# Kernel optimization log

Measured on AMD Instinct MI355X. Metric: run time of the kernel, lower is better.

Reference implementation:

```python
import jax, jax.numpy as jnp
import numpy as np

N_NODES = 100000
N_EDGES = 1600000
D = 128
N_CLASS = 10
N_LAYERS = 5
BN_EPS = 1e-5


def setup_inputs() -> dict:
    key = jax.random.key(0)
    ks = jax.random.split(key, 8)
    x = jax.random.normal(ks[0], (N_NODES, D), dtype=jnp.float32)
    edge_index = jax.random.randint(ks[1], (2, N_EDGES), 0, N_NODES, dtype=jnp.int32)
    s = 0.05  # small init scale for numerical stability through 5 layers
    W1 = jax.random.normal(ks[2], (N_LAYERS, D, D), dtype=jnp.float32) * s
    b1 = jnp.zeros((N_LAYERS, D), jnp.float32)
    gamma = jnp.ones((N_LAYERS, D), jnp.float32)
    beta = jnp.zeros((N_LAYERS, D), jnp.float32)
    mean = jnp.zeros((N_LAYERS, D), jnp.float32)
    var = jnp.ones((N_LAYERS, D), jnp.float32)
    W2 = jax.random.normal(ks[3], (N_LAYERS, D, D), dtype=jnp.float32) * s
    b2 = jnp.zeros((N_LAYERS, D), jnp.float32)
    lin1_w = jax.random.normal(ks[4], (D, D), dtype=jnp.float32) * s
    lin1_b = jnp.zeros((D,), jnp.float32)
    lin2_w = jax.random.normal(ks[5], (D, N_CLASS), dtype=jnp.float32) * s
    lin2_b = jnp.zeros((N_CLASS,), jnp.float32)
    return {"x": x, "edge_index": edge_index, "W1": W1, "b1": b1,
            "gamma": gamma, "beta": beta, "mean": mean, "var": var,
            "W2": W2, "b2": b2, "lin1_w": lin1_w, "lin1_b": lin1_b,
            "lin2_w": lin2_w, "lin2_b": lin2_b}


def reference(x, edge_index, W1, b1, gamma, beta, mean, var, W2, b2,
              lin1_w, lin1_b, lin2_w, lin2_b):
    n = x.shape[0]
    src, dst = edge_index[0], edge_index[1]
    h = x
    for l in range(N_LAYERS):
        # GIN aggregation: (1+eps)*h + sum_{j->i} h_j, eps=0 (GINConv default)
        agg = jax.ops.segment_sum(h[src], dst, num_segments=n)
        z = (h + agg) @ W1[l] + b1[l]
        # BatchNorm1d in eval mode (running stats)
        z = (z - mean[l]) * (gamma[l] / jnp.sqrt(var[l] + BN_EPS)) + beta[l]
        z = jax.nn.relu(z)
        h = jax.nn.relu(z @ W2[l] + b2[l])
    h = jax.nn.relu(h @ lin1_w + lin1_b)  # dropout is identity in eval
    h = h @ lin2_w + lin2_b
    return jax.nn.log_softmax(h, axis=1)
```

## Files before the change

### kernel.cpp

```cpp
#include <hip/hip_runtime.h>
#include <hip/hip_bf16.h>

#define DD 128
#define CAP 64

typedef __attribute__((ext_vector_type(8))) short short8;
typedef __attribute__((ext_vector_type(4))) float f32x4;

__device__ __forceinline__ float bf2f(short s) {
    union { unsigned u; float f; } c; c.u = ((unsigned)(unsigned short)s) << 16; return c.f;
}
__device__ __forceinline__ short f2bf(float f) {
    union { float f; unsigned u; } c; c.f = f;
    unsigned u = c.u + 0x7fffu + ((c.u >> 16) & 1u);
    return (short)(u >> 16);
}

__device__ __forceinline__ void gload_lds16(const void* g, void* l) {
    __builtin_amdgcn_global_load_lds(
        (const __attribute__((address_space(1))) unsigned int*)g,
        (__attribute__((address_space(3))) unsigned int*)l, 16, 0, 0);
}

__global__ __launch_bounds__(256) void f2b_k(
    const float* __restrict__ x, ushort* __restrict__ o, int n8)
{
    int i = blockIdx.x * 256 + threadIdx.x;
    if (i < n8) {
        float4 v0 = ((const float4*)x)[(size_t)i * 2];
        float4 v1 = ((const float4*)x)[(size_t)i * 2 + 1];
        short8 r;
        r[0] = f2bf(v0.x); r[1] = f2bf(v0.y); r[2] = f2bf(v0.z); r[3] = f2bf(v0.w);
        r[4] = f2bf(v1.x); r[5] = f2bf(v1.y); r[6] = f2bf(v1.z); r[7] = f2bf(v1.w);
        ((short8*)o)[i] = r;
    }
}

__global__ __launch_bounds__(256) void wconv_k(
    const float* __restrict__ W1, const float* __restrict__ W2,
    const float* __restrict__ L1, ushort* __restrict__ Wt)
{
    int idx = blockIdx.x * 256 + threadIdx.x;
    int mat = idx >> 14;
    if (mat >= 11) return;
    int e = idx & 16383;
    int k = e >> 7, n = e & 127;
    const float* src = (mat < 5) ? (W1 + (size_t)mat * 16384)
                     : (mat < 10) ? (W2 + (size_t)(mat - 5) * 16384) : L1;
    float v = src[e];
    int di = (n * 128 + k) ^ ((n & 7) << 3);
    Wt[(size_t)mat * 16384 + di] = (ushort)f2bf(v);
}

__global__ __launch_bounds__(256) void lin2conv_k(
    const float* __restrict__ w, ushort* __restrict__ L2t)
{
    int idx = blockIdx.x * 256 + threadIdx.x;
    if (idx >= 2048) return;
    int c = idx >> 7, k = idx & 127;
    float v = (c < 10) ? w[k * 10 + c] : 0.f;
    L2t[idx] = (ushort)f2bf(v);
}

#define RANGE_SUB 256
__global__ __launch_bounds__(256) void fill_k(
    const int* __restrict__ src, const int* __restrict__ dst,
    int* __restrict__ len, int* __restrict__ csr, int nEdges, int n)
{
    const int r    = blockIdx.x & 7;
    const int sub  = blockIdx.x >> 3;
    const int step = (n + 7) / 8;
    const int rlo  = r * step;
    const int rhi  = min(n, rlo + step);

    for (int base = sub * 1024; base < nEdges; base += RANGE_SUB * 1024) {
        int e0 = base + threadIdx.x * 4;
        if (e0 + 3 < nEdges) {
            int4 d = *(const int4*)(dst + e0);
            int4 s = *(const int4*)(src + e0);
            if (d.x >= rlo && d.x < rhi) { int i = atomicAdd(&len[d.x], 1); if (i < CAP) csr[(d.x << 6) + i] = s.x; }
            if (d.y >= rlo && d.y < rhi) { int i = atomicAdd(&len[d.y], 1); if (i < CAP) csr[(d.y << 6) + i] = s.y; }
            if (d.z >= rlo && d.z < rhi) { int i = atomicAdd(&len[d.z], 1); if (i < CAP) csr[(d.z << 6) + i] = s.z; }
            if (d.w >= rlo && d.w < rhi) { int i = atomicAdd(&len[d.w], 1); if (i < CAP) csr[(d.w << 6) + i] = s.w; }
        } else {
            for (int e = e0; e < nEdges; ++e) {
                int d = dst[e];
                if (d >= rlo && d < rhi) { int i = atomicAdd(&len[d], 1); if (i < CAP) csr[(d << 6) + i] = src[e]; }
            }
        }
    }
}

__global__ __launch_bounds__(256) void gather_bf_k(
    const ushort* __restrict__ h, const int* __restrict__ len,
    const int* __restrict__ csr, ushort* __restrict__ out, int n)
{
    int node = blockIdx.x * 16 + (threadIdx.x >> 4);
    int j = threadIdx.x & 15;
    if (node >= n) return;
    int beg = node << 6;
    int end = beg + min(len[node], CAP);
    const short8* hp = (const short8*)h;

    float a[8], b[8];
    short8 v = hp[(size_t)node * 16 + j];
#pragma unroll
    for (int i = 0; i < 8; ++i) { a[i] = bf2f(v[i]); b[i] = 0.f; }

    int k = beg;
    for (; k + 7 < end; k += 8) {
        int s0 = csr[k],     s1 = csr[k + 1], s2 = csr[k + 2], s3 = csr[k + 3];
        int s4 = csr[k + 4], s5 = csr[k + 5], s6 = csr[k + 6], s7 = csr[k + 7];
        short8 v0 = hp[(size_t)s0 * 16 + j];
        short8 v1 = hp[(size_t)s1 * 16 + j];
        short8 v2 = hp[(size_t)s2 * 16 + j];
        short8 v3 = hp[(size_t)s3 * 16 + j];
        short8 v4 = hp[(size_t)s4 * 16 + j];
        short8 v5 = hp[(size_t)s5 * 16 + j];
        short8 v6 = hp[(size_t)s6 * 16 + j];
        short8 v7 = hp[(size_t)s7 * 16 + j];
#pragma unroll
        for (int i = 0; i < 8; ++i) {
            a[i] += (bf2f(v0[i]) + bf2f(v1[i])) + (bf2f(v2[i]) + bf2f(v3[i]));
            b[i] += (bf2f(v4[i]) + bf2f(v5[i])) + (bf2f(v6[i]) + bf2f(v7[i]));
        }
    }
    if (k + 3 < end) {
        int s0 = csr[k], s1 = csr[k + 1], s2 = csr[k + 2], s3 = csr[k + 3];
        short8 v0 = hp[(size_t)s0 * 16 + j];
        short8 v1 = hp[(size_t)s1 * 16 + j];
        short8 v2 = hp[(size_t)s2 * 16 + j];
        short8 v3 = hp[(size_t)s3 * 16 + j];
#pragma unroll
        for (int i = 0; i < 8; ++i)
            a[i] += (bf2f(v0[i]) + bf2f(v1[i])) + (bf2f(v2[i]) + bf2f(v3[i]));
        k += 4;
    }
    for (; k < end; ++k) {
        int s0 = csr[k];
        short8 v0 = hp[(size_t)s0 * 16 + j];
#pragma unroll
        for (int i = 0; i < 8; ++i) b[i] += bf2f(v0[i]);
    }
    short8 r;
#pragma unroll
    for (int i = 0; i < 8; ++i) r[i] = f2bf(a[i] + b[i]);
    ((short8*)out)[(size_t)node * 16 + j] = r;
}

template <bool BN, int MODE>
__global__ __launch_bounds__(256, 2) void layer_k(
    const ushort* __restrict__ A, const ushort* __restrict__ W1t,
    const float* __restrict__ bias1,
    const float* __restrict__ gamma, const float* __restrict__ beta,
    const float* __restrict__ mean, const float* __restrict__ var,
    const ushort* __restrict__ W2t, const float* __restrict__ bias2,
    ushort* __restrict__ O, float* __restrict__ OUT, int nrows)
{
    __shared__ ushort sA[16384];
    __shared__ ushort sW[16384];
    const int tid  = threadIdx.x;
    const int row0 = blockIdx.x * 128;

    const int lane = tid & 63;
    const int wv   = tid >> 6;
    const int m0   = wv * 32;
    const int lr   = lane & 15;
    const int lg   = lane >> 4;

    short8 w2s[8];
    short8 b2f[4];
    if (MODE == 1) {
#pragma unroll
        for (int i = 0; i < 8; ++i)
            w2s[i] = ((const short8*)W2t)[i * 256 + tid];
    } else {
#pragma unroll
        for (int kk = 0; kk < 4; ++kk)
            b2f[kk] = *(const short8*)(W2t + lr * 128 + kk * 32 + lg * 8);
    }

#pragma unroll
    for (int i = 0; i < 8; ++i)
        gload_lds16(W1t + (i * 256 + tid) * 8, sW + (i * 256 + tid) * 8);
#pragma unroll
    for (int i = 0; i < 8; ++i) {
        int f  = i * 256 + tid;
        int r  = f >> 4;
        int c8 = f & 15;
        int gr = row0 + r;
        gload_lds16(A + (size_t)gr * DD + ((c8 ^ (r & 7)) * 8), sA + f * 8);
    }
    __syncthreads();

    float mul8[8], add8[8];
#pragma unroll
    for (int cf = 0; cf < 8; ++cf) {
        int n = cf * 16 + lr;
        if (BN) {
            float s = gamma[n] * rsqrtf(var[n] + 1e-5f);
            mul8[cf] = s;
            add8[cf] = (bias1[n] - mean[n]) * s + beta[n];
        } else {
            mul8[cf] = 1.f;
            add8[cf] = bias1[n];
        }
    }

    f32x4 acc[2][8];
#pragma unroll
    for (int rf = 0; rf < 2; ++rf)
#pragma unroll
        for (int cf = 0; cf < 8; ++cf) acc[rf][cf] = (f32x4){0.f, 0.f, 0.f, 0.f};

#pragma unroll
    for (int kk = 0; kk < 4; ++kk) {
        const int kb = kk * 64 + lg * 16;
        int ra0 = m0 + lr;
        int ra1 = m0 + 16 + lr;
        short8 a0 = *(short8*)((char*)sA + ((ra0 * 256 + kb) ^ ((ra0 & 7) << 4)));
        short8 a1 = *(short8*)((char*)sA + ((ra1 * 256 + kb) ^ ((ra1 & 7) << 4)));
        short8 b[8];
#pragma unroll
        for (int cf = 0; cf < 8; ++cf) {
            int rn = cf * 16 + lr;
            b[cf] = *(short8*)((char*)sW + ((rn * 256 + kb) ^ ((rn & 7) << 4)));
        }
#pragma unroll
        for (int cf = 0; cf < 8; ++cf) {
            acc[0][cf] = __builtin_amdgcn_mfma_f32_16x16x32_bf16(a0, b[cf], acc[0][cf], 0, 0, 0);
            acc[1][cf] = __builtin_amdgcn_mfma_f32_16x16x32_bf16(a1, b[cf], acc[1][cf], 0, 0, 0);
        }
    }

#pragma unroll
    for (int rf = 0; rf < 2; ++rf)
#pragma unroll
        for (int cf = 0; cf < 8; ++cf) {
            int n = cf * 16 + lr;
#pragma unroll
            for (int i = 0; i < 4; ++i) {
                int row = m0 + rf * 16 + lg * 4 + i;
                float vv = fmaxf(fmaf(acc[rf][cf][i], mul8[cf], add8[cf]), 0.f);
                int db = (row * 256 + n * 2) ^ ((row & 7) << 4);
                *(ushort*)((char*)sA + db) = (ushort)f2bf(vv);
            }
        }

    if (MODE == 1) {
        __syncthreads();
        {
            short8* dstv = (short8*)sW;
#pragma unroll
            for (int i = 0; i < 8; ++i) dstv[i * 256 + tid] = w2s[i];
        }
        __syncthreads();

        f32x4 acc2[2][8];
#pragma unroll
        for (int rf = 0; rf < 2; ++rf)
#pragma unroll
            for (int cf = 0; cf < 8; ++cf) acc2[rf][cf] = (f32x4){0.f, 0.f, 0.f, 0.f};

#pragma unroll
        for (int kk = 0; kk < 4; ++kk) {
            const int kb = kk * 64 + lg * 16;
            int ra0 = m0 + lr;
            int ra1 = m0 + 16 + lr;
            short8 a0 = *(short8*)((char*)sA + ((ra0 * 256 + kb) ^ ((ra0 & 7) << 4)));
            short8 a1 = *(short8*)((char*)sA + ((ra1 * 256 + kb) ^ ((ra1 & 7) << 4)));
            short8 b[8];
#pragma unroll
            for (int cf = 0; cf < 8; ++cf) {
                int rn = cf * 16 + lr;
                b[cf] = *(short8*)((char*)sW + ((rn * 256 + kb) ^ ((rn & 7) << 4)));
            }
#pragma unroll
            for (int cf = 0; cf < 8; ++cf) {
                acc2[0][cf] = __builtin_amdgcn_mfma_f32_16x16x32_bf16(a0, b[cf], acc2[0][cf], 0, 0, 0);
                acc2[1][cf] = __builtin_amdgcn_mfma_f32_16x16x32_bf16(a1, b[cf], acc2[1][cf], 0, 0, 0);
            }
        }

        float add2[8];
#pragma unroll
        for (int cf = 0; cf < 8; ++cf) add2[cf] = bias2[cf * 16 + lr];
#pragma unroll
        for (int rf = 0; rf < 2; ++rf)
#pragma unroll
            for (int cf = 0; cf < 8; ++cf) {
                int n = cf * 16 + lr;
#pragma unroll
                for (int i = 0; i < 4; ++i) {
                    int m = row0 + m0 + rf * 16 + lg * 4 + i;
                    if (m < nrows) {
                        float vv = fmaxf(acc2[rf][cf][i] + add2[cf], 0.f);
                        O[(size_t)m * DD + n] = (ushort)f2bf(vv);
                    }
                }
            }
    } else {
        f32x4 acc2[2];
        acc2[0] = (f32x4){0.f, 0.f, 0.f, 0.f};
        acc2[1] = (f32x4){0.f, 0.f, 0.f, 0.f};
#pragma unroll
        for (int kk = 0; kk < 4; ++kk) {
            const int kb = kk * 64 + lg * 16;
            int ra0 = m0 + lr;
            int ra1 = m0 + 16 + lr;
            short8 a0 = *(short8*)((char*)sA + ((ra0 * 256 + kb) ^ ((ra0 & 7) << 4)));
            short8 a1 = *(short8*)((char*)sA + ((ra1 * 256 + kb) ^ ((ra1 & 7) << 4)));
            acc2[0] = __builtin_amdgcn_mfma_f32_16x16x32_bf16(a0, b2f[kk], acc2[0], 0, 0, 0);
            acc2[1] = __builtin_amdgcn_mfma_f32_16x16x32_bf16(a1, b2f[kk], acc2[1], 0, 0, 0);
        }
        float bc = (lr < 10) ? bias2[lr] : 0.f;
#pragma unroll
        for (int rf = 0; rf < 2; ++rf) {
#pragma unroll
            for (int i = 0; i < 4; ++i) {
                float p = (lr < 10) ? (acc2[rf][i] + bc) : -__builtin_inff();
                float m = p;
#pragma unroll
                for (int off = 8; off >= 1; off >>= 1)
                    m = fmaxf(m, __shfl_xor(m, off, 64));
                float e = expf(p - m);
#pragma unroll
                for (int off = 8; off >= 1; off >>= 1)
                    e += __shfl_xor(e, off, 64);
                float lse = m + logf(e);
                int grow = row0 + m0 + rf * 16 + lg * 4 + i;
                if (lr < 10 && grow < nrows)
                    OUT[(size_t)grow * 10 + lr] = p - lse;
            }
        }
    }
}


extern "C" void kernel_launch(void* const* d_in, const int* in_sizes, int n_in,
                              void* d_out, int out_size, void* d_ws, size_t ws_size,
                              hipStream_t stream)
{
    const float* x      = (const float*)d_in[0];
    const int*   ei     = (const int*)d_in[1];
    const float* W1     = (const float*)d_in[2];
    const float* b1     = (const float*)d_in[3];
    const float* gamma  = (const float*)d_in[4];
    const float* beta   = (const float*)d_in[5];
    const float* mean   = (const float*)d_in[6];
    const float* var    = (const float*)d_in[7];
    const float* W2     = (const float*)d_in[8];
    const float* b2     = (const float*)d_in[9];
    const float* lin1_w = (const float*)d_in[10];
    const float* lin1_b = (const float*)d_in[11];
    const float* lin2_w = (const float*)d_in[12];
    const float* lin2_b = (const float*)d_in[13];

    const int N = in_sizes[0] / DD;
    const int E = in_sizes[1] / 2;
    const int* srcI = ei;
    const int* dstI = ei + E;

    ushort* hb  = (ushort*)d_ws;
    ushort* gb  = hb + (size_t)N * DD;
    ushort* Wt  = gb + (size_t)N * DD;
    ushort* L2t = Wt + 11 * 16384;
    int*    len = (int*)(L2t + 2048);
    int*    csr = len + N;

    const int gemmGrid = (N + 127) / 128;

    f2b_k<<<(N * DD / 8 + 255) / 256, 256, 0, stream>>>(x, hb, N * DD / 8);
    wconv_k<<<704, 256, 0, stream>>>(W1, W2, lin1_w, Wt);
    lin2conv_k<<<8, 256, 0, stream>>>(lin2_w, L2t);

    hipMemsetAsync(len, 0, (size_t)N * sizeof(int), stream);
    fill_k<<<8 * RANGE_SUB, 256, 0, stream>>>(srcI, dstI, len, csr, E, N);

    for (int l = 0; l < 5; ++l) {
        gather_bf_k<<<(N + 15) / 16, 256, 0, stream>>>(hb, len, csr, gb, N);
        layer_k<true, 1><<<gemmGrid, 256, 0, stream>>>(
            gb, Wt + (size_t)l * 16384, b1 + (size_t)l * DD,
            gamma + (size_t)l * DD, beta + (size_t)l * DD,
            mean + (size_t)l * DD, var + (size_t)l * DD,
            Wt + (size_t)(5 + l) * 16384, b2 + (size_t)l * DD, hb, nullptr, N);
    }
    layer_k<false, 2><<<gemmGrid, 256, 0, stream>>>(
        hb, Wt + (size_t)10 * 16384, lin1_b,
        nullptr, nullptr, nullptr, nullptr,
        L2t, lin2_b, nullptr, (float*)d_out, N);
}
```

Before: 536.1 us.

## Partition edges into destination-range buckets before building CSR adjacency

Replaces the CSR fill, where each of 8 range groups rescanned the entire edge list, with two passes. The first pass buckets every edge once by destination range into a packed buffer, using block-local counts and one global atomic per bucket. The second pass fills per-node slots from each bucket. This removes the 8x redundant reads of src/dst, but adds an extra kernel, a packed-buffer round trip, and a fixed bucket capacity that could overflow on skewed inputs.

```diff
diff --git a/kernel.cpp b/kernel.cpp
--- a/kernel.cpp
+++ b/kernel.cpp
@@ -62,32 +62,63 @@
     L2t[idx] = (ushort)f2bf(v);
 }
 
-#define RANGE_SUB 256
-__global__ __launch_bounds__(256) void fill_k(
+__global__ void initcur_k(int* __restrict__ gcur, int bcap)
+{
+    if (threadIdx.x < 8) gcur[threadIdx.x] = threadIdx.x * bcap;
+}
+
+__global__ __launch_bounds__(256) void parta_k(
     const int* __restrict__ src, const int* __restrict__ dst,
-    int* __restrict__ len, int* __restrict__ csr, int nEdges, int n)
+    int* __restrict__ gcur, int* __restrict__ ebuf, int nEdges, int n)
+{
+    __shared__ int cnt[8], base[8], rank[8];
+    const int step = (n + 7) / 8;
+    const int t = threadIdx.x;
+    if (t < 8) cnt[t] = 0;
+    __syncthreads();
+
+    int e0 = blockIdx.x * 1024 + t * 4;
+    int d4[4], s4[4], r4[4];
+    int m = 0;
+    if (e0 + 3 < nEdges) {
+        int4 d = *(const int4*)(dst + e0);
+        int4 s = *(const int4*)(src + e0);
+        d4[0] = d.x; d4[1] = d.y; d4[2] = d.z; d4[3] = d.w;
+        s4[0] = s.x; s4[1] = s.y; s4[2] = s.z; s4[3] = s.w;
+        m = 4;
+    } else {
+        for (int e = e0; e < nEdges; ++e) { d4[m] = dst[e]; s4[m] = src[e]; ++m; }
+    }
+    for (int i = 0; i < m; ++i) {
+        r4[i] = d4[i] / step;
+        atomicAdd(&cnt[r4[i]], 1);
+    }
+    __syncthreads();
+    if (t < 8) { base[t] = atomicAdd(&gcur[t], cnt[t]); rank[t] = 0; }
+    __syncthreads();
+    for (int i = 0; i < m; ++i) {
+        int r = r4[i];
+        int pos = base[r] + atomicAdd(&rank[r], 1);
+        ebuf[pos] = ((d4[i] - r * step) << 17) | s4[i];
+    }
+}
+
+#define FSUB 128
+__global__ __launch_bounds__(256) void fillb_k(
+    const int* __restrict__ ebuf, const int* __restrict__ gcur,
+    int* __restrict__ len, int* __restrict__ csr, int n, int bcap)
 {
     const int r    = blockIdx.x & 7;
     const int sub  = blockIdx.x >> 3;
     const int step = (n + 7) / 8;
     const int rlo  = r * step;
-    const int rhi  = min(n, rlo + step);
-
-    for (int base = sub * 1024; base < nEdges; base += RANGE_SUB * 1024) {
-        int e0 = base + threadIdx.x * 4;
-        if (e0 + 3 < nEdges) {
-            int4 d = *(const int4*)(dst + e0);
-            int4 s = *(const int4*)(src + e0);
-            if (d.x >= rlo && d.x < rhi) { int i = atomicAdd(&len[d.x], 1); if (i < CAP) csr[(d.x << 6) + i] = s.x; }
-            if (d.y >= rlo && d.y < rhi) { int i = atomicAdd(&len[d.y], 1); if (i < CAP) csr[(d.y << 6) + i] = s.y; }
-            if (d.z >= rlo && d.z < rhi) { int i = atomicAdd(&len[d.z], 1); if (i < CAP) csr[(d.z << 6) + i] = s.z; }
-            if (d.w >= rlo && d.w < rhi) { int i = atomicAdd(&len[d.w], 1); if (i < CAP) csr[(d.w << 6) + i] = s.w; }
-        } else {
-            for (int e = e0; e < nEdges; ++e) {
-                int d = dst[e];
-                if (d >= rlo && d < rhi) { int i = atomicAdd(&len[d], 1); if (i < CAP) csr[(d << 6) + i] = src[e]; }
-            }
-        }
+    const int end  = gcur[r];
+    for (int i = r * bcap + sub * 256 + threadIdx.x; i < end; i += FSUB * 256) {
+        unsigned p = (unsigned)ebuf[i];
+        int d = rlo + (int)(p >> 17);
+        int s = (int)(p & 0x1FFFFu);
+        int slot = atomicAdd(&len[d], 1);
+        if (slot < CAP) csr[(d << 6) + slot] = s;
     }
 }
 
@@ -361,12 +392,16 @@
     const int* srcI = ei;
     const int* dstI = ei + E;
 
-    ushort* hb  = (ushort*)d_ws;
-    ushort* gb  = hb + (size_t)N * DD;
-    ushort* Wt  = gb + (size_t)N * DD;
-    ushort* L2t = Wt + 11 * 16384;
-    int*    len = (int*)(L2t + 2048);
-    int*    csr = len + N;
+    const int bcap = E / 8 + 16384;
+
+    ushort* hb   = (ushort*)d_ws;
+    ushort* gb   = hb + (size_t)N * DD;
+    ushort* Wt   = gb + (size_t)N * DD;
+    ushort* L2t  = Wt + 11 * 16384;
+    int*    len  = (int*)(L2t + 2048);
+    int*    csr  = len + N;
+    int*    gcur = csr + (size_t)N * CAP;
+    int*    ebuf = gcur + 8;
 
     const int gemmGrid = (N + 127) / 128;
 
@@ -375,7 +410,9 @@
     lin2conv_k<<<8, 256, 0, stream>>>(lin2_w, L2t);
 
     hipMemsetAsync(len, 0, (size_t)N * sizeof(int), stream);
-    fill_k<<<8 * RANGE_SUB, 256, 0, stream>>>(srcI, dstI, len, csr, E, N);
+    initcur_k<<<1, 8, 0, stream>>>(gcur, bcap);
+    parta_k<<<(E + 1023) / 1024, 256, 0, stream>>>(srcI, dstI, gcur, ebuf, E, N);
+    fillb_k<<<8 * FSUB, 256, 0, stream>>>(ebuf, gcur, len, csr, N, bcap);
 
     for (int l = 0; l < 5; ++l) {
         gather_bf_k<<<(N + 15) / 16, 256, 0, stream>>>(hb, len, csr, gb, N);
```

Measured after the change: 554.3 us. +3.4%, slower.
